# Kernel tuning notes

Measured on AMD Instinct MI355X. Metric: run time of the kernel, lower is better.

The kernel has to match this reference:

```python
import jax, jax.numpy as jnp
import numpy as np

N = 100000   # nodes
E = 640000   # edges
IN = 256     # raw input feature dim
D = 128      # post-MLP node feature dim (fixed in FilterGNN)


def setup_inputs() -> dict:
    key = jax.random.key(0)
    ks = jax.random.split(key, 10)
    x = jax.random.normal(ks[0], (N, IN), jnp.float32)
    alpha = jax.random.uniform(ks[1], (E, 1), jnp.float32)  # edge gate logits in [0,1)
    edge_index = jax.random.randint(ks[2], (2, E), 0, N, dtype=jnp.int32)
    norm = jnp.ones((E,), jnp.float32)  # passed to message in the original but unused
    # MLP `lin`: in_channels -> 512 -> 256 -> 128 (kaiming-normal weights, zero bias)
    def kaiming(k, fan_out, fan_in):
        return jax.random.normal(k, (fan_out, fan_in), jnp.float32) * jnp.sqrt(2.0 / fan_in)
    W1 = kaiming(ks[3], 512, IN); b1 = jnp.zeros((512,), jnp.float32)
    W2 = kaiming(ks[4], 256, 512); b2 = jnp.zeros((256,), jnp.float32)
    W3 = kaiming(ks[5], D, 256);  b3 = jnp.zeros((D,), jnp.float32)
    return {"x": x, "alpha": alpha, "edge_index": edge_index, "norm": norm,
            "W1": W1, "b1": b1, "W2": W2, "b2": b2, "W3": W3, "b3": b3}


def reference(x, alpha, edge_index, norm, W1, b1, W2, b2, W3, b3):
    # FilterGNN.lin: Linear-Tanh-Linear-Tanh-Linear  -> [N, 128]
    h = jnp.tanh(x @ W1.T + b1)
    h = jnp.tanh(h @ W2.T + b2)
    h = h @ W3.T + b3
    # FilterGraphConv1: gather x_j, elementwise relu gate, scatter-mean over targets.
    # (The [-1, H, C] view with H*C = 128 is a pure reshape; the gate broadcasts
    #  over all features, so the math is identical without the head split.)
    src, dst = edge_index[0], edge_index[1]
    gate = 2.0 * jax.nn.relu(jax.lax.stop_gradient(alpha) - 0.5)  # [E, 1]
    msg = h[src] * gate                                           # [E, 128] gather + gate
    sums = jax.ops.segment_sum(msg, dst, num_segments=N)          # [N, 128]
    cnt = jax.ops.segment_sum(jnp.ones((E,), h.dtype), dst, num_segments=N)
    out = sums / jnp.maximum(cnt, 1.0)[:, None]                   # scatter-mean (0 if no edges)
    return out
```

## Files before the change

kernel.cpp:

```cpp
#include <hip/hip_runtime.h>

typedef __attribute__((ext_vector_type(8))) short short8;
typedef __attribute__((ext_vector_type(4))) float f32x4;

__device__ __forceinline__ unsigned short f2bf(float f) {
    union { float f; unsigned u; } v; v.f = f;
    unsigned r = v.u + 0x7FFFu + ((v.u >> 16) & 1u);
    return (unsigned short)(r >> 16);
}
__device__ __forceinline__ float bf2f(unsigned short h) {
    union { unsigned u; float f; } v; v.u = ((unsigned)h) << 16;
    return v.f;
}

__device__ __forceinline__ float tanh_fast(float x) {
    float xc = fminf(fmaxf(x, -9.0f), 9.0f);
    float t  = __expf(2.0f * xc);
    return (t - 1.0f) * __builtin_amdgcn_rcpf(t + 1.0f);
}

__device__ __forceinline__ unsigned long long pack4(float4 v) {
    return (unsigned long long)f2bf(v.x)
         | ((unsigned long long)f2bf(v.y) << 16)
         | ((unsigned long long)f2bf(v.z) << 32)
         | ((unsigned long long)f2bf(v.w) << 48);
}

#define GLD16(gptr, lptr)                                                     \
    __builtin_amdgcn_global_load_lds(                                         \
        (const __attribute__((address_space(1))) unsigned int*)(gptr),        \
        (__attribute__((address_space(3))) unsigned int*)(lptr), 16, 0, 0)

__global__ __launch_bounds__(256) void cast_w(
    const float* __restrict__ W1, unsigned short* __restrict__ w1bf,
    const float* __restrict__ W2, unsigned short* __restrict__ w2bf,
    const float* __restrict__ W3, unsigned short* __restrict__ w3bf)
{
    int t = blockIdx.x * 256 + threadIdx.x;
    const float* s; unsigned short* d; int q;
    if (t < 32768)      { s = W1; d = w1bf; q = t; }
    else if (t < 65536) { s = W2; d = w2bf; q = t - 32768; }
    else if (t < 73728) { s = W3; d = w3bf; q = t - 65536; }
    else return;
    int base = q * 4;
    float4 v = *(const float4*)(s + base);
    *(unsigned long long*)(d + base) = pack4(v);
}

__global__ __launch_bounds__(512, 2) void mlp_fused(
    const float* __restrict__ x,
    const unsigned short* __restrict__ W1, const float* __restrict__ b1,
    const unsigned short* __restrict__ W2, const float* __restrict__ b2,
    const unsigned short* __restrict__ W3, const float* __restrict__ b3,
    unsigned short* __restrict__ hout, int M)
{
    __shared__ __align__(16) short Bs[256][64];
    __shared__ __align__(16) short h1s[64][520];
    __shared__ __align__(16) short pool[64 * 264];

    const int tid  = threadIdx.x;
    const int wave = tid >> 6;
    const int lane = tid & 63;
    const int m0   = blockIdx.x * 64;
    const int wm   = (wave >> 1) * 16;
    const int half = wave & 1;
    const int lm   = lane & 15;
    const int quad = lane >> 4;
    const int srow = lane >> 3;
    const int scol = ((lane & 7) ^ srow) * 8;
    const int cc0  = (quad ^ (lm & 7)) * 8;
    const int cc1  = ((4 + quad) ^ (lm & 7)) * 8;

    short (*xs)[64]   = (short(*)[64])pool;
    short (*h2s)[264] = (short(*)[264])pool;

    {
        int gr = m0 + wave * 8 + srow; if (gr >= M) gr = M - 1;
        const float* xr = x + (size_t)gr * 256;
        #pragma unroll
        for (int kt = 0; kt < 4; ++kt) {
            float4 va = *(const float4*)(xr + kt * 64 + scol);
            float4 vb = *(const float4*)(xr + kt * 64 + scol + 4);
            unsigned long long* dp =
                (unsigned long long*)&xs[kt * 64 + wave * 8 + srow][(lane & 7) * 8];
            dp[0] = pack4(va); dp[1] = pack4(vb);
        }
    }

    for (int nh = 0; nh < 2; ++nh) {
        f32x4 acc[8] = {};
        for (int kt = 0; kt < 4; ++kt) {
            #pragma unroll
            for (int i = 0; i < 4; ++i) {
                int r0 = wave * 32 + i * 8;
                GLD16(W1 + (size_t)(nh * 256 + r0 + srow) * 256 + kt * 64 + scol, &Bs[r0][0]);
            }
            __syncthreads();
            #pragma unroll
            for (int ks = 0; ks < 2; ++ks) {
                const int cc = ks ? cc1 : cc0;
                short8 af = *(const short8*)&xs[kt * 64 + wm + lm][cc];
                #pragma unroll
                for (int in = 0; in < 8; ++in) {
                    short8 bv = *(const short8*)&Bs[half * 128 + in * 16 + lm][cc];
                    acc[in] = __builtin_amdgcn_mfma_f32_16x16x32_bf16(af, bv, acc[in], 0, 0, 0);
                }
            }
            __syncthreads();
        }
        int rb = wm + quad * 4;
        #pragma unroll
        for (int in = 0; in < 8; ++in) {
            int col = nh * 256 + half * 128 + in * 16 + lm;
            float bv = b1[col];
            #pragma unroll
            for (int r = 0; r < 4; ++r)
                h1s[rb + r][col] = (short)f2bf(tanh_fast(acc[in][r] + bv));
        }
    }
    __syncthreads();

    {
        f32x4 acc[8] = {};
        for (int k0 = 0; k0 < 512; k0 += 64) {
            #pragma unroll
            for (int i = 0; i < 4; ++i) {
                int r0 = wave * 32 + i * 8;
                GLD16(W2 + (size_t)(r0 + srow) * 512 + k0 + scol, &Bs[r0][0]);
            }
            __syncthreads();
            #pragma unroll
            for (int ks = 0; ks < 2; ++ks) {
                const int cc = ks ? cc1 : cc0;
                short8 af = *(const short8*)&h1s[wm + lm][k0 + ks * 32 + quad * 8];
                #pragma unroll
                for (int in = 0; in < 8; ++in) {
                    short8 bv = *(const short8*)&Bs[half * 128 + in * 16 + lm][cc];
                    acc[in] = __builtin_amdgcn_mfma_f32_16x16x32_bf16(af, bv, acc[in], 0, 0, 0);
                }
            }
            __syncthreads();
        }
        int rb = wm + quad * 4;
        #pragma unroll
        for (int in = 0; in < 8; ++in) {
            int col = half * 128 + in * 16 + lm;
            float bv = b2[col];
            #pragma unroll
            for (int r = 0; r < 4; ++r)
                h2s[rb + r][col] = (short)f2bf(tanh_fast(acc[in][r] + bv));
        }
    }

    {
        f32x4 acc[4] = {};
        for (int k0 = 0; k0 < 256; k0 += 64) {
            #pragma unroll
            for (int i = 0; i < 2; ++i) {
                int r0 = wave * 16 + i * 8;
                GLD16(W3 + (size_t)(r0 + srow) * 256 + k0 + scol, &Bs[r0][0]);
            }
            __syncthreads();
            #pragma unroll
            for (int ks = 0; ks < 2; ++ks) {
                const int cc = ks ? cc1 : cc0;
                short8 af = *(const short8*)&h2s[wm + lm][k0 + ks * 32 + quad * 8];
                #pragma unroll
                for (int in = 0; in < 4; ++in) {
                    short8 bv = *(const short8*)&Bs[half * 64 + in * 16 + lm][cc];
                    acc[in] = __builtin_amdgcn_mfma_f32_16x16x32_bf16(af, bv, acc[in], 0, 0, 0);
                }
            }
            __syncthreads();
        }
        int gm_base = m0 + wm + quad * 4;
        #pragma unroll
        for (int in = 0; in < 4; ++in) {
            int gn = half * 64 + in * 16 + lm;
            float bv = b3[gn];
            #pragma unroll
            for (int r = 0; r < 4; ++r) {
                int gm = gm_base + r;
                if (gm < M)
                    hout[(size_t)gm * 128 + gn] = f2bf(acc[in][r] + bv);
            }
        }
    }
}

__global__ __launch_bounds__(256) void edge_hist(
    const int* __restrict__ ei, const float* __restrict__ alpha,
    unsigned long long* __restrict__ deg, int E)
{
    int e = blockIdx.x * 256 + threadIdx.x;
    if (e >= E) return;
    int dst = ei[E + e];
    float gate = 2.0f * fmaxf(alpha[e] - 0.5f, 0.0f);
    atomicAdd(&deg[dst], 0x100000000ULL | (gate > 0.0f ? 1ULL : 0ULL));
}

__global__ __launch_bounds__(256) void scan1(
    const unsigned long long* __restrict__ deg, int* __restrict__ rowptr,
    int* __restrict__ cursor, int* __restrict__ partials, int N)
{
    __shared__ int sums[256];
    int base = blockIdx.x * 1024 + threadIdx.x * 4;
    int v[4];
    #pragma unroll
    for (int i = 0; i < 4; ++i) {
        int idx = base + i;
        v[i] = (idx < N) ? (int)(deg[idx] & 0xffffffffULL) : 0;
    }
    int s = v[0] + v[1] + v[2] + v[3];
    sums[threadIdx.x] = s;
    __syncthreads();
    for (int off = 1; off < 256; off <<= 1) {
        int t = (threadIdx.x >= off) ? sums[threadIdx.x - off] : 0;
        __syncthreads();
        sums[threadIdx.x] += t;
        __syncthreads();
    }
    int excl = sums[threadIdx.x] - s;
    if (threadIdx.x == 255) partials[blockIdx.x] = sums[255];
    int run = excl;
    #pragma unroll
    for (int i = 0; i < 4; ++i) {
        int idx = base + i;
        if (idx < N) { rowptr[idx] = run; cursor[idx] = run; }
        run += v[i];
    }
}

__global__ __launch_bounds__(256) void scan2(int* __restrict__ partials, int nb)
{
    __shared__ int s[256];
    int v = (threadIdx.x < nb) ? partials[threadIdx.x] : 0;
    s[threadIdx.x] = v;
    __syncthreads();
    for (int off = 1; off < 256; off <<= 1) {
        int t = (threadIdx.x >= off) ? s[threadIdx.x - off] : 0;
        __syncthreads();
        s[threadIdx.x] += t;
        __syncthreads();
    }
    partials[threadIdx.x] = s[threadIdx.x] - v;
}

__global__ __launch_bounds__(256) void edge_fill(
    const int* __restrict__ ei, const float* __restrict__ alpha,
    int* __restrict__ cursor, const int* __restrict__ partials,
    int2* __restrict__ recs, int E)
{
    int e = blockIdx.x * 256 + threadIdx.x;
    if (e >= E) return;
    float gate = 2.0f * fmaxf(alpha[e] - 0.5f, 0.0f);
    if (gate > 0.0f) {
        int dst = ei[E + e];
        int src = ei[e];
        int pos = atomicAdd(&cursor[dst], 1) + partials[dst >> 10];
        recs[pos] = make_int2(src, __float_as_int(gate));
    }
}

__global__ __launch_bounds__(256) void node_gather(
    const unsigned short* __restrict__ h, const unsigned long long* __restrict__ deg,
    const int* __restrict__ rowptr, const int* __restrict__ partials,
    const int2* __restrict__ recs, float* __restrict__ out, int N)
{
    int wave = threadIdx.x >> 6;
    int lane = threadIdx.x & 63;
    int node = blockIdx.x * 4 + wave;
    if (node >= N) return;
    unsigned long long d = deg[node];
    int dAll  = __builtin_amdgcn_readfirstlane((int)(d >> 32));
    int dG    = __builtin_amdgcn_readfirstlane((int)(d & 0xffffffffULL));
    int start = __builtin_amdgcn_readfirstlane(rowptr[node] + partials[node >> 10]);
    int qw = lane >> 4, ql = lane & 15;
    float a[8] = {};
    for (int j = 0; j < dG; j += 4) {
        int jj = j + qw;
        int idx = start + (jj < dG ? jj : dG - 1);
        int2 rec = recs[idx];
        float gate = (jj < dG) ? __int_as_float(rec.y) : 0.0f;
        uint4 u = *(const uint4*)(h + ((size_t)rec.x << 7) + ql * 8);
        a[0] += bf2f((unsigned short)(u.x & 0xffffu)) * gate;
        a[1] += bf2f((unsigned short)(u.x >> 16)) * gate;
        a[2] += bf2f((unsigned short)(u.y & 0xffffu)) * gate;
        a[3] += bf2f((unsigned short)(u.y >> 16)) * gate;
        a[4] += bf2f((unsigned short)(u.z & 0xffffu)) * gate;
        a[5] += bf2f((unsigned short)(u.z >> 16)) * gate;
        a[6] += bf2f((unsigned short)(u.w & 0xffffu)) * gate;
        a[7] += bf2f((unsigned short)(u.w >> 16)) * gate;
    }
    #pragma unroll
    for (int i = 0; i < 8; ++i) {
        a[i] += __shfl_xor(a[i], 16);
        a[i] += __shfl_xor(a[i], 32);
    }
    if (qw == 0) {
        float inv = 1.0f / fmaxf((float)dAll, 1.0f);
        float* op = out + ((size_t)node << 7) + ql * 8;
        *(float4*)(op)     = make_float4(a[0] * inv, a[1] * inv, a[2] * inv, a[3] * inv);
        *(float4*)(op + 4) = make_float4(a[4] * inv, a[5] * inv, a[6] * inv, a[7] * inv);
    }
}

extern "C" void kernel_launch(void* const* d_in, const int* in_sizes, int n_in,
                              void* d_out, int out_size, void* d_ws, size_t ws_size,
                              hipStream_t stream) {
    const float* x     = (const float*)d_in[0];
    const float* alpha = (const float*)d_in[1];
    const int*   ei    = (const int*)d_in[2];
    const float* W1 = (const float*)d_in[4];
    const float* b1 = (const float*)d_in[5];
    const float* W2 = (const float*)d_in[6];
    const float* b2 = (const float*)d_in[7];
    const float* W3 = (const float*)d_in[8];
    const float* b3 = (const float*)d_in[9];
    float* out = (float*)d_out;

    const int N = in_sizes[0] / 256;
    const int E = in_sizes[1];
    const int H1 = 512, D = 128;

    char* ws = (char*)d_ws;
    size_t off = 0;
    auto take = [&](size_t bytes) { char* p = ws + off; off = (off + bytes + 255) & ~(size_t)255; return p; };
    unsigned short* hbf  = (unsigned short*)take((size_t)N * D  * 2);
    unsigned short* w1bf = (unsigned short*)take((size_t)H1 * 256 * 2);
    unsigned short* w2bf = (unsigned short*)take((size_t)256 * H1 * 2);
    unsigned short* w3bf = (unsigned short*)take((size_t)D * 256 * 2);
    unsigned long long* deg = (unsigned long long*)take((size_t)N * 8);
    int*  rowptr   = (int*)take((size_t)N * 4);
    int*  cursor   = (int*)take((size_t)N * 4);
    int*  partials = (int*)take(256 * 4);
    int2* recs     = (int2*)take((size_t)E * 8);

    dim3 blk(256);

    cast_w<<<288, blk, 0, stream>>>(W1, w1bf, W2, w2bf, W3, w3bf);
    mlp_fused<<<(N + 63) / 64, dim3(512), 0, stream>>>(
        x, w1bf, b1, w2bf, b2, w3bf, b3, hbf, N);

    hipMemsetAsync(deg, 0, (size_t)N * 8, stream);
    edge_hist<<<(E + 255) / 256, blk, 0, stream>>>(ei, alpha, deg, E);
    const int nb1 = (N + 1023) / 1024;
    scan1<<<nb1, blk, 0, stream>>>(deg, rowptr, cursor, partials, N);
    scan2<<<1, blk, 0, stream>>>(partials, nb1);
    edge_fill<<<(E + 255) / 256, blk, 0, stream>>>(ei, alpha, cursor, partials, recs, E);

    node_gather<<<(N + 3) / 4, blk, 0, stream>>>(hbf, deg, rowptr, partials, recs, out, N);
}
```

Before: 414.7 us.

## Double-buffer weight tiles across MLP layers and swizzle hidden activations in LDS

Doubles the LDS weight buffer so each k-step prefetches the next W1/W2/W3 tile, including across layer boundaries, while MFMAs run on the current tile. This cuts the syncs per k-step from two to one. The padded h1s/h2s activation arrays are replaced with unpadded arrays that use an XOR column swizzle to avoid bank conflicts. The aim is to hide global-to-LDS weight load latency and remove sync stalls, at the cost of more LDS per block (about 160KB total) and heavier unrolled code.

```diff
diff --git a/kernel.cpp b/kernel.cpp
--- a/kernel.cpp
+++ b/kernel.cpp
@@ -54,9 +54,9 @@
     const unsigned short* __restrict__ W3, const float* __restrict__ b3,
     unsigned short* __restrict__ hout, int M)
 {
-    __shared__ __align__(16) short Bs[256][64];
-    __shared__ __align__(16) short h1s[64][520];
-    __shared__ __align__(16) short pool[64 * 264];
+    __shared__ __align__(16) short Bs[2][256][64];
+    __shared__ __align__(16) short h1s[64 * 512];
+    __shared__ __align__(16) short pool[64 * 256];
 
     const int tid  = threadIdx.x;
     const int wave = tid >> 6;
@@ -70,9 +70,32 @@
     const int scol = ((lane & 7) ^ srow) * 8;
     const int cc0  = (quad ^ (lm & 7)) * 8;
     const int cc1  = ((4 + quad) ^ (lm & 7)) * 8;
-
-    short (*xs)[64]   = (short(*)[64])pool;
-    short (*h2s)[264] = (short(*)[264])pool;
+    const int swzA = (lm & 7) << 3;
+
+    short (*xs)[64] = (short(*)[64])pool;
+    short* h2s      = pool;
+
+    auto stage_w1 = [&](int nh, int kt, int b) {
+        #pragma unroll
+        for (int i = 0; i < 4; ++i) {
+            int r0 = wave * 32 + i * 8;
+            GLD16(W1 + (size_t)(nh * 256 + r0 + srow) * 256 + kt * 64 + scol, &Bs[b][r0][0]);
+        }
+    };
+    auto stage_w2 = [&](int kt, int b) {
+        #pragma unroll
+        for (int i = 0; i < 4; ++i) {
+            int r0 = wave * 32 + i * 8;
+            GLD16(W2 + (size_t)(r0 + srow) * 512 + kt * 64 + scol, &Bs[b][r0][0]);
+        }
+    };
+    auto stage_w3 = [&](int kt, int b) {
+        #pragma unroll
+        for (int i = 0; i < 2; ++i) {
+            int r0 = wave * 16 + i * 8;
+            GLD16(W3 + (size_t)(r0 + srow) * 256 + kt * 64 + scol, &Bs[b][r0][0]);
+        }
+    };
 
     {
         int gr = m0 + wave * 8 + srow; if (gr >= M) gr = M - 1;
@@ -86,92 +109,104 @@
             dp[0] = pack4(va); dp[1] = pack4(vb);
         }
     }
-
+    stage_w1(0, 0, 0);
+    __syncthreads();
+
+    #pragma unroll
     for (int nh = 0; nh < 2; ++nh) {
         f32x4 acc[8] = {};
+        #pragma unroll
         for (int kt = 0; kt < 4; ++kt) {
-            #pragma unroll
-            for (int i = 0; i < 4; ++i) {
-                int r0 = wave * 32 + i * 8;
-                GLD16(W1 + (size_t)(nh * 256 + r0 + srow) * 256 + kt * 64 + scol, &Bs[r0][0]);
-            }
-            __syncthreads();
+            const int s = nh * 4 + kt;
+            if (s < 7) stage_w1((s + 1) >> 2, (s + 1) & 3, (s + 1) & 1);
+            else       stage_w2(0, 0);
+            short (*bs)[64] = Bs[s & 1];
             #pragma unroll
             for (int ks = 0; ks < 2; ++ks) {
                 const int cc = ks ? cc1 : cc0;
                 short8 af = *(const short8*)&xs[kt * 64 + wm + lm][cc];
                 #pragma unroll
                 for (int in = 0; in < 8; ++in) {
-                    short8 bv = *(const short8*)&Bs[half * 128 + in * 16 + lm][cc];
+                    short8 bv = *(const short8*)&bs[half * 128 + in * 16 + lm][cc];
                     acc[in] = __builtin_amdgcn_mfma_f32_16x16x32_bf16(af, bv, acc[in], 0, 0, 0);
                 }
             }
+            if (kt == 3) {
+                int rb = wm + quad * 4;
+                #pragma unroll
+                for (int in = 0; in < 8; ++in) {
+                    int col = nh * 256 + half * 128 + in * 16 + lm;
+                    float bv = b1[col];
+                    #pragma unroll
+                    for (int r = 0; r < 4; ++r) {
+                        int row = rb + r;
+                        h1s[row * 512 + (col ^ ((row & 7) << 3))] =
+                            (short)f2bf(tanh_fast(acc[in][r] + bv));
+                    }
+                }
+            }
             __syncthreads();
         }
-        int rb = wm + quad * 4;
-        #pragma unroll
-        for (int in = 0; in < 8; ++in) {
-            int col = nh * 256 + half * 128 + in * 16 + lm;
-            float bv = b1[col];
-            #pragma unroll
-            for (int r = 0; r < 4; ++r)
-                h1s[rb + r][col] = (short)f2bf(tanh_fast(acc[in][r] + bv));
-        }
-    }
-    __syncthreads();
+    }
 
     {
         f32x4 acc[8] = {};
-        for (int k0 = 0; k0 < 512; k0 += 64) {
-            #pragma unroll
-            for (int i = 0; i < 4; ++i) {
-                int r0 = wave * 32 + i * 8;
-                GLD16(W2 + (size_t)(r0 + srow) * 512 + k0 + scol, &Bs[r0][0]);
-            }
-            __syncthreads();
+        #pragma unroll
+        for (int kt = 0; kt < 8; ++kt) {
+            const int s = 8 + kt;
+            if (kt < 7) stage_w2(kt + 1, (s + 1) & 1);
+            else        stage_w3(0, (s + 1) & 1);
+            short (*bs)[64] = Bs[s & 1];
             #pragma unroll
             for (int ks = 0; ks < 2; ++ks) {
                 const int cc = ks ? cc1 : cc0;
-                short8 af = *(const short8*)&h1s[wm + lm][k0 + ks * 32 + quad * 8];
+                const int row = wm + lm;
+                const int base = kt * 64 + ks * 32 + quad * 8;
+                short8 af = *(const short8*)&h1s[row * 512 + (base ^ swzA)];
                 #pragma unroll
                 for (int in = 0; in < 8; ++in) {
-                    short8 bv = *(const short8*)&Bs[half * 128 + in * 16 + lm][cc];
+                    short8 bv = *(const short8*)&bs[half * 128 + in * 16 + lm][cc];
                     acc[in] = __builtin_amdgcn_mfma_f32_16x16x32_bf16(af, bv, acc[in], 0, 0, 0);
                 }
             }
+            if (kt == 7) {
+                int rb = wm + quad * 4;
+                #pragma unroll
+                for (int in = 0; in < 8; ++in) {
+                    int col = half * 128 + in * 16 + lm;
+                    float bv = b2[col];
+                    #pragma unroll
+                    for (int r = 0; r < 4; ++r) {
+                        int row = rb + r;
+                        h2s[row * 256 + (col ^ ((row & 7) << 3))] =
+                            (short)f2bf(tanh_fast(acc[in][r] + bv));
+                    }
+                }
+            }
             __syncthreads();
-        }
-        int rb = wm + quad * 4;
-        #pragma unroll
-        for (int in = 0; in < 8; ++in) {
-            int col = half * 128 + in * 16 + lm;
-            float bv = b2[col];
-            #pragma unroll
-            for (int r = 0; r < 4; ++r)
-                h2s[rb + r][col] = (short)f2bf(tanh_fast(acc[in][r] + bv));
         }
     }
 
     {
         f32x4 acc[4] = {};
-        for (int k0 = 0; k0 < 256; k0 += 64) {
-            #pragma unroll
-            for (int i = 0; i < 2; ++i) {
-                int r0 = wave * 16 + i * 8;
-                GLD16(W3 + (size_t)(r0 + srow) * 256 + k0 + scol, &Bs[r0][0]);
-            }
-            __syncthreads();
+        #pragma unroll
+        for (int kt = 0; kt < 4; ++kt) {
+            const int s = 16 + kt;
+            if (kt < 3) stage_w3(kt + 1, (s + 1) & 1);
+            short (*bs)[64] = Bs[s & 1];
             #pragma unroll
             for (int ks = 0; ks < 2; ++ks) {
                 const int cc = ks ? cc1 : cc0;
-                short8 af = *(const short8*)&h2s[wm + lm][k0 + ks * 32 + quad * 8];
+                const int row = wm + lm;
+                const int base = kt * 64 + ks * 32 + quad * 8;
+                short8 af = *(const short8*)&h2s[row * 256 + (base ^ swzA)];
                 #pragma unroll
                 for (int in = 0; in < 4; ++in) {
-                    short8 bv = *(const short8*)&Bs[half * 64 + in * 16 + lm][cc];
+                    short8 bv = *(const short8*)&bs[half * 64 + in * 16 + lm][cc];
                     acc[in] = __builtin_amdgcn_mfma_f32_16x16x32_bf16(af, bv, acc[in], 0, 0, 0);
                 }
             }
-            __syncthreads();
+            if (kt < 3) __syncthreads();
         }
         int gm_base = m0 + wm + quad * 4;
         #pragma unroll
```

Result: slower. 429.1 us (+3.5%).

## Restructure fused MLP to read weights directly from global and shrink LDS

Applied to the files above, without the earlier changes.

The fused three-layer MLP kernel no longer stages weight tiles into LDS with global_load_lds. Each wave now loads its own slice of output columns straight from global memory (expected to be L2-resident) and computes all 64 rows of the block, so activation fragments are reused across four row tiles. LDS shrinks to an x buffer and a single h1/h2 buffer with XOR swizzling, and launch bounds rise from 2 to 4 blocks per CU. This removes most barriers and LDS weight traffic in exchange for more global and L2 weight reads per block and higher register pressure.

```diff
diff --git a/kernel.cpp b/kernel.cpp
--- a/kernel.cpp
+++ b/kernel.cpp
@@ -25,11 +25,6 @@
          | ((unsigned long long)f2bf(v.z) << 32)
          | ((unsigned long long)f2bf(v.w) << 48);
 }
-
-#define GLD16(gptr, lptr)                                                     \
-    __builtin_amdgcn_global_load_lds(                                         \
-        (const __attribute__((address_space(1))) unsigned int*)(gptr),        \
-        (__attribute__((address_space(3))) unsigned int*)(lptr), 16, 0, 0)
 
 __global__ __launch_bounds__(256) void cast_w(
     const float* __restrict__ W1, unsigned short* __restrict__ w1bf,
@@ -47,142 +42,159 @@
     *(unsigned long long*)(d + base) = pack4(v);
 }
 
-__global__ __launch_bounds__(512, 2) void mlp_fused(
+__global__ __launch_bounds__(512, 4) void mlp_fused(
     const float* __restrict__ x,
     const unsigned short* __restrict__ W1, const float* __restrict__ b1,
     const unsigned short* __restrict__ W2, const float* __restrict__ b2,
     const unsigned short* __restrict__ W3, const float* __restrict__ b3,
     unsigned short* __restrict__ hout, int M)
 {
-    __shared__ __align__(16) short Bs[256][64];
-    __shared__ __align__(16) short h1s[64][520];
-    __shared__ __align__(16) short pool[64 * 264];
+    __shared__ __align__(16) short xs[64 * 128];
+    __shared__ __align__(16) short h1s[64 * 512];
 
     const int tid  = threadIdx.x;
     const int wave = tid >> 6;
     const int lane = tid & 63;
     const int m0   = blockIdx.x * 64;
-    const int wm   = (wave >> 1) * 16;
-    const int half = wave & 1;
     const int lm   = lane & 15;
     const int quad = lane >> 4;
-    const int srow = lane >> 3;
-    const int scol = ((lane & 7) ^ srow) * 8;
-    const int cc0  = (quad ^ (lm & 7)) * 8;
-    const int cc1  = ((4 + quad) ^ (lm & 7)) * 8;
-
-    short (*xs)[64]   = (short(*)[64])pool;
-    short (*h2s)[264] = (short(*)[264])pool;
+    const int axor = (lm & 7) << 3;
+
+    const int srow = wave * 8 + (lane >> 3);
+    const int sl   = (lane & 7) * 8;
+    const int sxor = (srow & 7) << 3;
+
+    int gr = m0 + srow; if (gr >= M) gr = M - 1;
+    const float* xr = x + (size_t)gr * 256;
+
+    auto stage_x = [&](int kh) {
+        const float* p = xr + kh * 128;
+        float4 a0 = *(const float4*)(p + sl);
+        float4 a1 = *(const float4*)(p + sl + 4);
+        float4 c0 = *(const float4*)(p + 64 + sl);
+        float4 c1 = *(const float4*)(p + 64 + sl + 4);
+        unsigned long long* d0 = (unsigned long long*)&xs[srow * 128 + (sl ^ sxor)];
+        d0[0] = pack4(a0); d0[1] = pack4(a1);
+        unsigned long long* d1 = (unsigned long long*)&xs[srow * 128 + 64 + (sl ^ sxor)];
+        d1[0] = pack4(c0); d1[1] = pack4(c1);
+    };
 
     {
-        int gr = m0 + wave * 8 + srow; if (gr >= M) gr = M - 1;
-        const float* xr = x + (size_t)gr * 256;
+        const int w64 = wave * 64;
+        f32x4 acc[4][4] = {};
+        stage_x(0);
+        __syncthreads();
+        #pragma unroll
+        for (int kh = 0; kh < 2; ++kh) {
+            if (kh == 1) { __syncthreads(); stage_x(1); __syncthreads(); }
+            #pragma unroll
+            for (int kt = 0; kt < 2; ++kt) {
+                #pragma unroll
+                for (int ks = 0; ks < 2; ++ks) {
+                    const int klocal = kt * 64 + ks * 32 + quad * 8;
+                    const int kglob  = kh * 128 + klocal;
+                    short8 af[4], bv[4];
+                    #pragma unroll
+                    for (int rm = 0; rm < 4; ++rm)
+                        af[rm] = *(const short8*)&xs[(rm * 16 + lm) * 128 +
+                                     (klocal & 64) + ((klocal & 63) ^ axor)];
+                    #pragma unroll
+                    for (int in = 0; in < 4; ++in)
+                        bv[in] = *(const short8*)&W1[(size_t)(w64 + in * 16 + lm) * 256 + kglob];
+                    #pragma unroll
+                    for (int rm = 0; rm < 4; ++rm)
+                        #pragma unroll
+                        for (int in = 0; in < 4; ++in)
+                            acc[rm][in] = __builtin_amdgcn_mfma_f32_16x16x32_bf16(
+                                af[rm], bv[in], acc[rm][in], 0, 0, 0);
+                }
+            }
+        }
+        #pragma unroll
+        for (int in = 0; in < 4; ++in) {
+            float bb = b1[w64 + in * 16 + lm];
+            #pragma unroll
+            for (int rm = 0; rm < 4; ++rm) {
+                #pragma unroll
+                for (int r = 0; r < 4; ++r) {
+                    int row = rm * 16 + quad * 4 + r;
+                    h1s[row * 512 + w64 + ((in * 16 + lm) ^ ((row & 7) << 3))] =
+                        (short)f2bf(tanh_fast(acc[rm][in][r] + bb));
+                }
+            }
+        }
+    }
+    __syncthreads();
+
+    short* h2s = h1s;
+    {
+        const int w32 = wave * 32;
+        f32x4 acc[4][2] = {};
+        #pragma unroll
+        for (int kt = 0; kt < 8; ++kt) {
+            #pragma unroll
+            for (int ks = 0; ks < 2; ++ks) {
+                const int col = kt * 64 + ks * 32 + quad * 8;
+                short8 af[4], bv[2];
+                #pragma unroll
+                for (int rm = 0; rm < 4; ++rm)
+                    af[rm] = *(const short8*)&h1s[(rm * 16 + lm) * 512 +
+                                 (col & 0x1C0) + ((col & 63) ^ axor)];
+                #pragma unroll
+                for (int in = 0; in < 2; ++in)
+                    bv[in] = *(const short8*)&W2[(size_t)(w32 + in * 16 + lm) * 512 + col];
+                #pragma unroll
+                for (int rm = 0; rm < 4; ++rm)
+                    #pragma unroll
+                    for (int in = 0; in < 2; ++in)
+                        acc[rm][in] = __builtin_amdgcn_mfma_f32_16x16x32_bf16(
+                            af[rm], bv[in], acc[rm][in], 0, 0, 0);
+            }
+        }
+        __syncthreads();
+        #pragma unroll
+        for (int in = 0; in < 2; ++in) {
+            float bb = b2[w32 + in * 16 + lm];
+            #pragma unroll
+            for (int rm = 0; rm < 4; ++rm) {
+                #pragma unroll
+                for (int r = 0; r < 4; ++r) {
+                    int row = rm * 16 + quad * 4 + r;
+                    int col = w32 + in * 16 + lm;
+                    h2s[row * 256 + (col & 0xC0) + ((col & 63) ^ ((row & 7) << 3))] =
+                        (short)f2bf(tanh_fast(acc[rm][in][r] + bb));
+                }
+            }
+        }
+    }
+    __syncthreads();
+
+    {
+        const int w16 = wave * 16;
+        f32x4 acc[4] = {};
         #pragma unroll
         for (int kt = 0; kt < 4; ++kt) {
-            float4 va = *(const float4*)(xr + kt * 64 + scol);
-            float4 vb = *(const float4*)(xr + kt * 64 + scol + 4);
-            unsigned long long* dp =
-                (unsigned long long*)&xs[kt * 64 + wave * 8 + srow][(lane & 7) * 8];
-            dp[0] = pack4(va); dp[1] = pack4(vb);
-        }
-    }
-
-    for (int nh = 0; nh < 2; ++nh) {
-        f32x4 acc[8] = {};
-        for (int kt = 0; kt < 4; ++kt) {
-            #pragma unroll
-            for (int i = 0; i < 4; ++i) {
-                int r0 = wave * 32 + i * 8;
-                GLD16(W1 + (size_t)(nh * 256 + r0 + srow) * 256 + kt * 64 + scol, &Bs[r0][0]);
-            }
-            __syncthreads();
             #pragma unroll
             for (int ks = 0; ks < 2; ++ks) {
-                const int cc = ks ? cc1 : cc0;
-                short8 af = *(const short8*)&xs[kt * 64 + wm + lm][cc];
-                #pragma unroll
-                for (int in = 0; in < 8; ++in) {
-                    short8 bv = *(const short8*)&Bs[half * 128 + in * 16 + lm][cc];
-                    acc[in] = __builtin_amdgcn_mfma_f32_16x16x32_bf16(af, bv, acc[in], 0, 0, 0);
+                const int col = kt * 64 + ks * 32 + quad * 8;
+                short8 bv = *(const short8*)&W3[(size_t)(w16 + lm) * 256 + col];
+                #pragma unroll
+                for (int rm = 0; rm < 4; ++rm) {
+                    short8 af = *(const short8*)&h2s[(rm * 16 + lm) * 256 +
+                                    (col & 0xC0) + ((col & 63) ^ axor)];
+                    acc[rm] = __builtin_amdgcn_mfma_f32_16x16x32_bf16(
+                        af, bv, acc[rm], 0, 0, 0);
                 }
             }
-            __syncthreads();
-        }
-        int rb = wm + quad * 4;
-        #pragma unroll
-        for (int in = 0; in < 8; ++in) {
-            int col = nh * 256 + half * 128 + in * 16 + lm;
-            float bv = b1[col];
-            #pragma unroll
-            for (int r = 0; r < 4; ++r)
-                h1s[rb + r][col] = (short)f2bf(tanh_fast(acc[in][r] + bv));
-        }
-    }
-    __syncthreads();
-
-    {
-        f32x4 acc[8] = {};
-        for (int k0 = 0; k0 < 512; k0 += 64) {
-            #pragma unroll
-            for (int i = 0; i < 4; ++i) {
-                int r0 = wave * 32 + i * 8;
-                GLD16(W2 + (size_t)(r0 + srow) * 512 + k0 + scol, &Bs[r0][0]);
-            }
-            __syncthreads();
-            #pragma unroll
-            for (int ks = 0; ks < 2; ++ks) {
-                const int cc = ks ? cc1 : cc0;
-                short8 af = *(const short8*)&h1s[wm + lm][k0 + ks * 32 + quad * 8];
-                #pragma unroll
-                for (int in = 0; in < 8; ++in) {
-                    short8 bv = *(const short8*)&Bs[half * 128 + in * 16 + lm][cc];
-                    acc[in] = __builtin_amdgcn_mfma_f32_16x16x32_bf16(af, bv, acc[in], 0, 0, 0);
-                }
-            }
-            __syncthreads();
-        }
-        int rb = wm + quad * 4;
-        #pragma unroll
-        for (int in = 0; in < 8; ++in) {
-            int col = half * 128 + in * 16 + lm;
-            float bv = b2[col];
-            #pragma unroll
-            for (int r = 0; r < 4; ++r)
-                h2s[rb + r][col] = (short)f2bf(tanh_fast(acc[in][r] + bv));
-        }
-    }
-
-    {
-        f32x4 acc[4] = {};
-        for (int k0 = 0; k0 < 256; k0 += 64) {
-            #pragma unroll
-            for (int i = 0; i < 2; ++i) {
-                int r0 = wave * 16 + i * 8;
-                GLD16(W3 + (size_t)(r0 + srow) * 256 + k0 + scol, &Bs[r0][0]);
-            }
-            __syncthreads();
-            #pragma unroll
-            for (int ks = 0; ks < 2; ++ks) {
-                const int cc = ks ? cc1 : cc0;
-                short8 af = *(const short8*)&h2s[wm + lm][k0 + ks * 32 + quad * 8];
-                #pragma unroll
-                for (int in = 0; in < 4; ++in) {
-                    short8 bv = *(const short8*)&Bs[half * 64 + in * 16 + lm][cc];
-                    acc[in] = __builtin_amdgcn_mfma_f32_16x16x32_bf16(af, bv, acc[in], 0, 0, 0);
-                }
-            }
-            __syncthreads();
-        }
-        int gm_base = m0 + wm + quad * 4;
-        #pragma unroll
-        for (int in = 0; in < 4; ++in) {
-            int gn = half * 64 + in * 16 + lm;
-            float bv = b3[gn];
+        }
+        float bb = b3[w16 + lm];
+        #pragma unroll
+        for (int rm = 0; rm < 4; ++rm) {
             #pragma unroll
             for (int r = 0; r < 4; ++r) {
-                int gm = gm_base + r;
+                int gm = m0 + rm * 16 + quad * 4 + r;
                 if (gm < M)
-                    hout[(size_t)gm * 128 + gn] = f2bf(acc[in][r] + bv);
+                    hout[(size_t)gm * 128 + w16 + lm] = f2bf(acc[rm][r] + bb);
             }
         }
     }
```

After: 396.6 us. 1.05x faster.
